# Optimization experiments

Hardware: AMD Instinct MI355X
Metric: run time of the kernel (lower is better)

Reference implementation:

```python
import jax, jax.numpy as jnp
import numpy as np

N_LAYERS, N_POS, D_MODEL, D_TC = 8, 1024, 768, 4096


def setup_inputs() -> dict:
    key = jax.random.key(0)
    ks = jax.random.split(key, 5)
    x = jax.random.normal(ks[0], (N_LAYERS, N_POS, D_MODEL), dtype=jnp.float32)
    W_enc = jax.random.normal(ks[1], (N_LAYERS, D_TC, D_MODEL), dtype=jnp.float32) * 0.02
    b_enc = jax.random.normal(ks[2], (N_LAYERS, D_TC), dtype=jnp.float32) * 0.02
    # Packed triangular decoder: W_dec[i, j] is the decoder from source layer i
    # writing into destination layer j (valid only for j >= i; rest is masked out).
    W_dec = jax.random.normal(ks[3], (N_LAYERS, N_LAYERS, D_TC, D_MODEL), dtype=jnp.float32) * 0.02
    b_dec = jax.random.normal(ks[4], (N_LAYERS, D_MODEL), dtype=jnp.float32) * 0.02
    return {"x": x, "W_enc": W_enc, "b_enc": b_enc, "W_dec": W_dec, "b_dec": b_dec}


def reference(x, W_enc, b_enc, W_dec, b_dec):
    # Encode: per-layer dense projection + ReLU (sparsity-inducing nonlinearity)
    feats = jax.nn.relu(jnp.einsum('lbd,lfd->lbf', x, W_enc) + b_enc[:, None, :])
    # Triangular cross-layer decode: source layer i writes to all layers j >= i
    L = W_dec.shape[0]
    tri = (jnp.arange(L)[:, None] <= jnp.arange(L)[None, :]).astype(W_dec.dtype)
    recon = jnp.einsum('ibf,ijfd->jbd', feats, W_dec * tri[:, :, None, None])
    recon = recon + b_dec[:, None, :]
    return recon
```

## Files before the change

kernel.cpp:

```cpp
#include <hip/hip_runtime.h>

#define NL 8
#define NP 1024
#define DM 768
#define FT 4096

typedef short bf16x8 __attribute__((ext_vector_type(8)));
typedef float f32x4  __attribute__((ext_vector_type(4)));
typedef unsigned short u16;

static __device__ __forceinline__ u16 f2bf(float f) {
    union { float f; unsigned int u; } c; c.f = f;
    unsigned int u = c.u;
    u += 0x7fffu + ((u >> 16) & 1u);
    return (u16)(u >> 16);
}

__global__ __launch_bounds__(256) void cvt_bf16_k(const float* __restrict__ in,
                                                  u16* __restrict__ out, int n8) {
    int i = blockIdx.x * 256 + threadIdx.x;
    if (i >= n8) return;
    const f32x4* p = (const f32x4*)in + (size_t)2 * i;
    f32x4 a = p[0], b = p[1];
    bf16x8 v;
    v[0] = (short)f2bf(a[0]); v[1] = (short)f2bf(a[1]);
    v[2] = (short)f2bf(a[2]); v[3] = (short)f2bf(a[3]);
    v[4] = (short)f2bf(b[0]); v[5] = (short)f2bf(b[1]);
    v[6] = (short)f2bf(b[2]); v[7] = (short)f2bf(b[3]);
    *((bf16x8*)out + i) = v;
}

__global__ __launch_bounds__(256) void init_out_k(float* __restrict__ out,
                                                  const float* __restrict__ bdec) {
    int i = blockIdx.x * 256 + threadIdx.x;
    int e = i * 4;
    int d = e % DM;
    int j = e / (NP * DM);
    f32x4 v = *(const f32x4*)(bdec + j * DM + d);
    *(f32x4*)(out + e) = v;
}

__global__ __launch_bounds__(256, 2) void encode_gemm(const u16* __restrict__ xb,
                                                      const u16* __restrict__ wb,
                                                      const float* __restrict__ benc,
                                                      u16* __restrict__ feats) {
    __shared__ u16 Al[128 * 40];
    __shared__ u16 Bl[128 * 40];
    const int l  = blockIdx.y;
    const int mt = blockIdx.x >> 5;
    const int nt = blockIdx.x & 31;
    const int m0 = mt * 128, n0 = nt * 128;
    const int t = threadIdx.x;
    const int lane = t & 63, w = t >> 6;
    const int lm = lane & 15, q = lane >> 4;
    const int wm = w >> 1, wn = w & 1;

    const u16* Ag = xb + (size_t)l * NP * DM + (size_t)(m0 + (t >> 1)) * DM + (t & 1) * 16;
    const u16* Bg = wb + (size_t)l * FT * DM + (size_t)(n0 + (t >> 1)) * DM + (t & 1) * 16;
    u16* Aw = &Al[(t >> 1) * 40 + (t & 1) * 16];
    u16* Bw = &Bl[(t >> 1) * 40 + (t & 1) * 16];

    f32x4 acc[4][4];
#pragma unroll
    for (int a = 0; a < 4; ++a)
#pragma unroll
        for (int b = 0; b < 4; ++b) acc[a][b] = (f32x4){0.f, 0.f, 0.f, 0.f};

    for (int k0 = 0; k0 < DM; k0 += 32) {
        bf16x8 a0 = *(const bf16x8*)(Ag + k0);
        bf16x8 a1 = *(const bf16x8*)(Ag + k0 + 8);
        bf16x8 b0 = *(const bf16x8*)(Bg + k0);
        bf16x8 b1 = *(const bf16x8*)(Bg + k0 + 8);
        __syncthreads();
        *(bf16x8*)Aw = a0; *(bf16x8*)(Aw + 8) = a1;
        *(bf16x8*)Bw = b0; *(bf16x8*)(Bw + 8) = b1;
        __syncthreads();
        bf16x8 af[4], bfr[4];
#pragma unroll
        for (int a = 0; a < 4; ++a)
            af[a] = *(const bf16x8*)(&Al[(wm * 64 + a * 16 + lm) * 40 + q * 8]);
#pragma unroll
        for (int b = 0; b < 4; ++b)
            bfr[b] = *(const bf16x8*)(&Bl[(wn * 64 + b * 16 + lm) * 40 + q * 8]);
#pragma unroll
        for (int a = 0; a < 4; ++a)
#pragma unroll
            for (int b = 0; b < 4; ++b)
                acc[a][b] = __builtin_amdgcn_mfma_f32_16x16x32_bf16(af[a], bfr[b], acc[a][b], 0, 0, 0);
    }

#pragma unroll
    for (int a = 0; a < 4; ++a) {
        int mrow = m0 + wm * 64 + a * 16 + q * 4;
#pragma unroll
        for (int b = 0; b < 4; ++b) {
            int ncol = n0 + wn * 64 + b * 16 + lm;
            float bias = benc[l * FT + ncol];
#pragma unroll
            for (int r = 0; r < 4; ++r) {
                float v = acc[a][b][r] + bias;
                v = v > 0.f ? v : 0.f;
                feats[(size_t)l * NP * FT + (size_t)(mrow + r) * FT + ncol] = f2bf(v);
            }
        }
    }
}

__global__ __launch_bounds__(256, 2) void decode_gemm(const u16* __restrict__ feats,
                                                      const float* __restrict__ wdec,
                                                      float* __restrict__ out) {
    __shared__ u16 Al[128 * 40];
    __shared__ u16 Bl[128 * 40];
    const int p = blockIdx.y;
    int j = 0;
    while ((j + 1) * (j + 2) / 2 <= p) ++j;
    const int i = p - j * (j + 1) / 2;
    const int mt = blockIdx.x / 6, nt = blockIdx.x % 6;
    const int m0 = mt * 128, n0 = nt * 128;
    const int t = threadIdx.x;
    const int lane = t & 63, w = t >> 6;
    const int lm = lane & 15, q = lane >> 4;
    const int wm = w >> 1, wn = w & 1;

    const u16*  Ag = feats + (size_t)i * NP * FT + (size_t)(m0 + (t >> 1)) * FT + (t & 1) * 16;
    const float* Bg = wdec + (size_t)(i * NL + j) * FT * DM + n0 + (t & 127);
    const int khalf = (t >> 7) * 16;
    u16* Aw = &Al[(t >> 1) * 40 + (t & 1) * 16];
    u16* Bw = &Bl[(t & 127) * 40 + khalf];

    f32x4 acc[4][4];
#pragma unroll
    for (int a = 0; a < 4; ++a)
#pragma unroll
        for (int b = 0; b < 4; ++b) acc[a][b] = (f32x4){0.f, 0.f, 0.f, 0.f};

    for (int k0 = 0; k0 < FT; k0 += 32) {
        bf16x8 a0 = *(const bf16x8*)(Ag + k0);
        bf16x8 a1 = *(const bf16x8*)(Ag + k0 + 8);
        float v[16];
#pragma unroll
        for (int kk = 0; kk < 16; ++kk)
            v[kk] = Bg[(size_t)(k0 + khalf + kk) * DM];
        __syncthreads();
        *(bf16x8*)Aw = a0; *(bf16x8*)(Aw + 8) = a1;
        bf16x8 h0, h1;
#pragma unroll
        for (int kk = 0; kk < 8; ++kk) { h0[kk] = (short)f2bf(v[kk]); h1[kk] = (short)f2bf(v[8 + kk]); }
        *(bf16x8*)Bw = h0; *(bf16x8*)(Bw + 8) = h1;
        __syncthreads();
        bf16x8 af[4], bfr[4];
#pragma unroll
        for (int a = 0; a < 4; ++a)
            af[a] = *(const bf16x8*)(&Al[(wm * 64 + a * 16 + lm) * 40 + q * 8]);
#pragma unroll
        for (int b = 0; b < 4; ++b)
            bfr[b] = *(const bf16x8*)(&Bl[(wn * 64 + b * 16 + lm) * 40 + q * 8]);
#pragma unroll
        for (int a = 0; a < 4; ++a)
#pragma unroll
            for (int b = 0; b < 4; ++b)
                acc[a][b] = __builtin_amdgcn_mfma_f32_16x16x32_bf16(af[a], bfr[b], acc[a][b], 0, 0, 0);
    }

#pragma unroll
    for (int a = 0; a < 4; ++a) {
        int mrow = m0 + wm * 64 + a * 16 + q * 4;
#pragma unroll
        for (int b = 0; b < 4; ++b) {
            int ncol = n0 + wn * 64 + b * 16 + lm;
#pragma unroll
            for (int r = 0; r < 4; ++r)
                atomicAdd(out + (size_t)j * NP * DM + (size_t)(mrow + r) * DM + ncol, acc[a][b][r]);
        }
    }
}

extern "C" void kernel_launch(void* const* d_in, const int* in_sizes, int n_in,
                              void* d_out, int out_size, void* d_ws, size_t ws_size,
                              hipStream_t stream) {
    const float* x     = (const float*)d_in[0];
    const float* W_enc = (const float*)d_in[1];
    const float* b_enc = (const float*)d_in[2];
    const float* W_dec = (const float*)d_in[3];
    const float* b_dec = (const float*)d_in[4];
    float* out = (float*)d_out;

    u16* xb    = (u16*)d_ws;
    u16* wb    = xb + (size_t)NL * NP * DM;
    u16* feats = wb + (size_t)NL * FT * DM;

    cvt_bf16_k<<<(NL * NP * DM / 8 + 255) / 256, 256, 0, stream>>>(x, xb, NL * NP * DM / 8);
    cvt_bf16_k<<<(NL * FT * DM / 8 + 255) / 256, 256, 0, stream>>>(W_enc, wb, NL * FT * DM / 8);
    init_out_k<<<(NL * NP * DM / 4) / 256, 256, 0, stream>>>(out, b_dec);
    encode_gemm<<<dim3(256, 8), 256, 0, stream>>>(xb, wb, b_enc, feats);
    decode_gemm<<<dim3(48, 36), 256, 0, stream>>>(feats, W_dec, out);
}
```

Before: 1.647 ms.

## Pre-transpose decoder weights to bf16 and use direct global-to-LDS loads with 256x128 tiles

Adds a kernel that transposes and converts the 36 used decoder weight blocks to bf16 in K-major layout. This removes the strided per-element fp32 loads and in-loop conversion from the decode GEMM. Both GEMMs now load A and B tiles with global_load_lds straight into unpadded LDS and use larger 256x128 tiles with 4x8 MFMA per wave. The LDS layout has no padding, so fragment reads may hit bank conflicts. There is also an extra full pass over W_dec and more workspace, and the grids get smaller.

```diff
diff --git a/kernel.cpp b/kernel.cpp
--- a/kernel.cpp
+++ b/kernel.cpp
@@ -14,6 +14,12 @@
     unsigned int u = c.u;
     u += 0x7fffu + ((u >> 16) & 1u);
     return (u16)(u >> 16);
+}
+
+static __device__ __forceinline__ void gload_lds16(const u16* g, u16* l) {
+    __builtin_amdgcn_global_load_lds(
+        (const __attribute__((address_space(1))) unsigned int*)g,
+        (__attribute__((address_space(3))) unsigned int*)l, 16, 0, 0);
 }
 
 __global__ __launch_bounds__(256) void cvt_bf16_k(const float* __restrict__ in,
@@ -40,137 +46,173 @@
     *(f32x4*)(out + e) = v;
 }
 
+__global__ __launch_bounds__(256) void wdec_transpose(const float* __restrict__ wdec,
+                                                      u16* __restrict__ wt) {
+    __shared__ float Tl[64 * 65];
+    const int p = blockIdx.y;
+    int j = 0;
+    while ((j + 1) * (j + 2) / 2 <= p) ++j;
+    const int i = p - j * (j + 1) / 2;
+    const int tx = blockIdx.x & 63;
+    const int ty = blockIdx.x >> 6;
+    const int f0 = tx * 64, d0 = ty * 64;
+    const int t = threadIdx.x;
+
+    const float* src = wdec + (size_t)(i * NL + j) * FT * DM;
+    const int fl = t >> 4;
+    const int dl = (t & 15) * 4;
+#pragma unroll
+    for (int r = 0; r < 4; ++r) {
+        int f = fl + r * 16;
+        f32x4 v = *(const f32x4*)(src + (size_t)(f0 + f) * DM + d0 + dl);
+#pragma unroll
+        for (int c = 0; c < 4; ++c) Tl[(dl + c) * 65 + f] = v[c];
+    }
+    __syncthreads();
+    const int dr = t >> 2;
+    const int fo = (t & 3) * 16;
+    bf16x8 h0, h1;
+#pragma unroll
+    for (int c = 0; c < 8; ++c) {
+        h0[c] = (short)f2bf(Tl[dr * 65 + fo + c]);
+        h1[c] = (short)f2bf(Tl[dr * 65 + fo + 8 + c]);
+    }
+    u16* dst = wt + (size_t)p * DM * FT + (size_t)(d0 + dr) * FT + f0 + fo;
+    *(bf16x8*)dst = h0;
+    *(bf16x8*)(dst + 8) = h1;
+}
+
 __global__ __launch_bounds__(256, 2) void encode_gemm(const u16* __restrict__ xb,
                                                       const u16* __restrict__ wb,
                                                       const float* __restrict__ benc,
                                                       u16* __restrict__ feats) {
-    __shared__ u16 Al[128 * 40];
-    __shared__ u16 Bl[128 * 40];
+    __shared__ u16 Al[256 * 32];
+    __shared__ u16 Bl[128 * 32];
     const int l  = blockIdx.y;
     const int mt = blockIdx.x >> 5;
     const int nt = blockIdx.x & 31;
-    const int m0 = mt * 128, n0 = nt * 128;
-    const int t = threadIdx.x;
-    const int lane = t & 63, w = t >> 6;
+    const int m0 = mt * 256, n0 = nt * 128;
+    const int t = threadIdx.x, lane = t & 63, w = t >> 6;
     const int lm = lane & 15, q = lane >> 4;
-    const int wm = w >> 1, wn = w & 1;
-
-    const u16* Ag = xb + (size_t)l * NP * DM + (size_t)(m0 + (t >> 1)) * DM + (t & 1) * 16;
-    const u16* Bg = wb + (size_t)l * FT * DM + (size_t)(n0 + (t >> 1)) * DM + (t & 1) * 16;
-    u16* Aw = &Al[(t >> 1) * 40 + (t & 1) * 16];
-    u16* Bw = &Bl[(t >> 1) * 40 + (t & 1) * 16];
-
-    f32x4 acc[4][4];
+    const int r16 = lane >> 2, kq = (lane & 3) * 8;
+
+    const u16* Abase = xb + (size_t)l * NP * DM;
+    const u16* Bbase = wb + (size_t)l * FT * DM;
+
+    f32x4 acc[4][8];
 #pragma unroll
     for (int a = 0; a < 4; ++a)
 #pragma unroll
-        for (int b = 0; b < 4; ++b) acc[a][b] = (f32x4){0.f, 0.f, 0.f, 0.f};
+        for (int b = 0; b < 8; ++b) acc[a][b] = (f32x4){0.f, 0.f, 0.f, 0.f};
 
     for (int k0 = 0; k0 < DM; k0 += 32) {
-        bf16x8 a0 = *(const bf16x8*)(Ag + k0);
-        bf16x8 a1 = *(const bf16x8*)(Ag + k0 + 8);
-        bf16x8 b0 = *(const bf16x8*)(Bg + k0);
-        bf16x8 b1 = *(const bf16x8*)(Bg + k0 + 8);
-        __syncthreads();
-        *(bf16x8*)Aw = a0; *(bf16x8*)(Aw + 8) = a1;
-        *(bf16x8*)Bw = b0; *(bf16x8*)(Bw + 8) = b1;
-        __syncthreads();
-        bf16x8 af[4], bfr[4];
-#pragma unroll
-        for (int a = 0; a < 4; ++a)
-            af[a] = *(const bf16x8*)(&Al[(wm * 64 + a * 16 + lm) * 40 + q * 8]);
-#pragma unroll
-        for (int b = 0; b < 4; ++b)
-            bfr[b] = *(const bf16x8*)(&Bl[(wn * 64 + b * 16 + lm) * 40 + q * 8]);
-#pragma unroll
-        for (int a = 0; a < 4; ++a)
-#pragma unroll
-            for (int b = 0; b < 4; ++b)
+#pragma unroll
+        for (int s = 0; s < 4; ++s) {
+            int c = w + 4 * s;
+            gload_lds16(Abase + (size_t)(m0 + c * 16 + r16) * DM + k0 + kq,
+                        &Al[c * 512 + lane * 8]);
+        }
+#pragma unroll
+        for (int s = 0; s < 2; ++s) {
+            int c = w + 4 * s;
+            gload_lds16(Bbase + (size_t)(n0 + c * 16 + r16) * DM + k0 + kq,
+                        &Bl[c * 512 + lane * 8]);
+        }
+        __syncthreads();
+        bf16x8 af[4], bfr[8];
+#pragma unroll
+        for (int a = 0; a < 4; ++a)
+            af[a] = *(const bf16x8*)(&Al[(w * 64 + a * 16 + lm) * 32 + q * 8]);
+#pragma unroll
+        for (int b = 0; b < 8; ++b)
+            bfr[b] = *(const bf16x8*)(&Bl[(b * 16 + lm) * 32 + q * 8]);
+#pragma unroll
+        for (int a = 0; a < 4; ++a)
+#pragma unroll
+            for (int b = 0; b < 8; ++b)
                 acc[a][b] = __builtin_amdgcn_mfma_f32_16x16x32_bf16(af[a], bfr[b], acc[a][b], 0, 0, 0);
+        __syncthreads();
     }
 
 #pragma unroll
     for (int a = 0; a < 4; ++a) {
-        int mrow = m0 + wm * 64 + a * 16 + q * 4;
-#pragma unroll
-        for (int b = 0; b < 4; ++b) {
-            int ncol = n0 + wn * 64 + b * 16 + lm;
-            float bias = benc[l * FT + ncol];
+        int mr = m0 + w * 64 + a * 16 + q * 4;
+#pragma unroll
+        for (int b = 0; b < 8; ++b) {
+            int nc = n0 + b * 16 + lm;
+            float bias = benc[l * FT + nc];
 #pragma unroll
             for (int r = 0; r < 4; ++r) {
                 float v = acc[a][b][r] + bias;
                 v = v > 0.f ? v : 0.f;
-                feats[(size_t)l * NP * FT + (size_t)(mrow + r) * FT + ncol] = f2bf(v);
+                feats[(size_t)l * NP * FT + (size_t)(mr + r) * FT + nc] = f2bf(v);
             }
         }
     }
 }
 
 __global__ __launch_bounds__(256, 2) void decode_gemm(const u16* __restrict__ feats,
-                                                      const float* __restrict__ wdec,
+                                                      const u16* __restrict__ wt,
                                                       float* __restrict__ out) {
-    __shared__ u16 Al[128 * 40];
-    __shared__ u16 Bl[128 * 40];
+    __shared__ u16 Al[256 * 32];
+    __shared__ u16 Bl[128 * 32];
     const int p = blockIdx.y;
     int j = 0;
     while ((j + 1) * (j + 2) / 2 <= p) ++j;
     const int i = p - j * (j + 1) / 2;
     const int mt = blockIdx.x / 6, nt = blockIdx.x % 6;
-    const int m0 = mt * 128, n0 = nt * 128;
-    const int t = threadIdx.x;
-    const int lane = t & 63, w = t >> 6;
+    const int m0 = mt * 256, n0 = nt * 128;
+    const int t = threadIdx.x, lane = t & 63, w = t >> 6;
     const int lm = lane & 15, q = lane >> 4;
-    const int wm = w >> 1, wn = w & 1;
-
-    const u16*  Ag = feats + (size_t)i * NP * FT + (size_t)(m0 + (t >> 1)) * FT + (t & 1) * 16;
-    const float* Bg = wdec + (size_t)(i * NL + j) * FT * DM + n0 + (t & 127);
-    const int khalf = (t >> 7) * 16;
-    u16* Aw = &Al[(t >> 1) * 40 + (t & 1) * 16];
-    u16* Bw = &Bl[(t & 127) * 40 + khalf];
-
-    f32x4 acc[4][4];
+    const int r16 = lane >> 2, kq = (lane & 3) * 8;
+
+    const u16* Abase = feats + (size_t)i * NP * FT;
+    const u16* Bbase = wt + (size_t)p * DM * FT;
+
+    f32x4 acc[4][8];
 #pragma unroll
     for (int a = 0; a < 4; ++a)
 #pragma unroll
-        for (int b = 0; b < 4; ++b) acc[a][b] = (f32x4){0.f, 0.f, 0.f, 0.f};
+        for (int b = 0; b < 8; ++b) acc[a][b] = (f32x4){0.f, 0.f, 0.f, 0.f};
 
     for (int k0 = 0; k0 < FT; k0 += 32) {
-        bf16x8 a0 = *(const bf16x8*)(Ag + k0);
-        bf16x8 a1 = *(const bf16x8*)(Ag + k0 + 8);
-        float v[16];
-#pragma unroll
-        for (int kk = 0; kk < 16; ++kk)
-            v[kk] = Bg[(size_t)(k0 + khalf + kk) * DM];
-        __syncthreads();
-        *(bf16x8*)Aw = a0; *(bf16x8*)(Aw + 8) = a1;
-        bf16x8 h0, h1;
-#pragma unroll
-        for (int kk = 0; kk < 8; ++kk) { h0[kk] = (short)f2bf(v[kk]); h1[kk] = (short)f2bf(v[8 + kk]); }
-        *(bf16x8*)Bw = h0; *(bf16x8*)(Bw + 8) = h1;
-        __syncthreads();
-        bf16x8 af[4], bfr[4];
-#pragma unroll
-        for (int a = 0; a < 4; ++a)
-            af[a] = *(const bf16x8*)(&Al[(wm * 64 + a * 16 + lm) * 40 + q * 8]);
-#pragma unroll
-        for (int b = 0; b < 4; ++b)
-            bfr[b] = *(const bf16x8*)(&Bl[(wn * 64 + b * 16 + lm) * 40 + q * 8]);
-#pragma unroll
-        for (int a = 0; a < 4; ++a)
-#pragma unroll
-            for (int b = 0; b < 4; ++b)
+#pragma unroll
+        for (int s = 0; s < 4; ++s) {
+            int c = w + 4 * s;
+            gload_lds16(Abase + (size_t)(m0 + c * 16 + r16) * FT + k0 + kq,
+                        &Al[c * 512 + lane * 8]);
+        }
+#pragma unroll
+        for (int s = 0; s < 2; ++s) {
+            int c = w + 4 * s;
+            gload_lds16(Bbase + (size_t)(n0 + c * 16 + r16) * FT + k0 + kq,
+                        &Bl[c * 512 + lane * 8]);
+        }
+        __syncthreads();
+        bf16x8 af[4], bfr[8];
+#pragma unroll
+        for (int a = 0; a < 4; ++a)
+            af[a] = *(const bf16x8*)(&Al[(w * 64 + a * 16 + lm) * 32 + q * 8]);
+#pragma unroll
+        for (int b = 0; b < 8; ++b)
+            bfr[b] = *(const bf16x8*)(&Bl[(b * 16 + lm) * 32 + q * 8]);
+#pragma unroll
+        for (int a = 0; a < 4; ++a)
+#pragma unroll
+            for (int b = 0; b < 8; ++b)
                 acc[a][b] = __builtin_amdgcn_mfma_f32_16x16x32_bf16(af[a], bfr[b], acc[a][b], 0, 0, 0);
+        __syncthreads();
     }
 
 #pragma unroll
     for (int a = 0; a < 4; ++a) {
-        int mrow = m0 + wm * 64 + a * 16 + q * 4;
-#pragma unroll
-        for (int b = 0; b < 4; ++b) {
-            int ncol = n0 + wn * 64 + b * 16 + lm;
+        int mr = m0 + w * 64 + a * 16 + q * 4;
+#pragma unroll
+        for (int b = 0; b < 8; ++b) {
+            int nc = n0 + b * 16 + lm;
 #pragma unroll
             for (int r = 0; r < 4; ++r)
-                atomicAdd(out + (size_t)j * NP * DM + (size_t)(mrow + r) * DM + ncol, acc[a][b][r]);
+                atomicAdd(out + (size_t)j * NP * DM + (size_t)(mr + r) * DM + nc, acc[a][b][r]);
         }
     }
 }
@@ -188,10 +230,12 @@
     u16* xb    = (u16*)d_ws;
     u16* wb    = xb + (size_t)NL * NP * DM;
     u16* feats = wb + (size_t)NL * FT * DM;
+    u16* wt    = feats + (size_t)NL * NP * FT;
 
     cvt_bf16_k<<<(NL * NP * DM / 8 + 255) / 256, 256, 0, stream>>>(x, xb, NL * NP * DM / 8);
     cvt_bf16_k<<<(NL * FT * DM / 8 + 255) / 256, 256, 0, stream>>>(W_enc, wb, NL * FT * DM / 8);
     init_out_k<<<(NL * NP * DM / 4) / 256, 256, 0, stream>>>(out, b_dec);
-    encode_gemm<<<dim3(256, 8), 256, 0, stream>>>(xb, wb, b_enc, feats);
-    decode_gemm<<<dim3(48, 36), 256, 0, stream>>>(feats, W_dec, out);
-}
+    wdec_transpose<<<dim3(768, 36), 256, 0, stream>>>(W_dec, wt);
+    encode_gemm<<<dim3(128, 8), 256, 0, stream>>>(xb, wb, b_enc, feats);
+    decode_gemm<<<dim3(24, 36), 256, 0, stream>>>(feats, wt, out);
+}
```

Result: faster. 1.533 ms (-6.9%).
